# Kernel tuning notes

Hardware: AMD Instinct MI355X
Metric: run time of the kernel (lower is better)

The kernel has to match this reference:

```python
import jax, jax.numpy as jnp
import numpy as np

DIM = 768
N_HEADS = 12
HEAD_DIM = DIM // N_HEADS
MLP_MULT = 4
EPS = 1e-5


def setup_inputs() -> dict:
    key = jax.random.key(0)
    ks = jax.random.split(key, 8)
    B, T = 2, 4096
    s = lambda fan_in: 1.0 / np.sqrt(fan_in)
    return {
        "x": jax.random.normal(ks[0], (B, T, DIM), dtype=jnp.float32),
        "ln1_w": jnp.ones((DIM,), jnp.float32),
        "ln1_b": jnp.zeros((DIM,), jnp.float32),
        # weights stored as (in, out): y = x @ W + b (equivalent to torch Linear)
        "w_qkv": jax.random.normal(ks[1], (DIM, 3 * DIM), jnp.float32) * s(DIM),
        "w_proj": jax.random.normal(ks[2], (DIM, DIM), jnp.float32) * s(DIM),
        "b_proj": jnp.zeros((DIM,), jnp.float32),
        "ln2_w": jnp.ones((DIM,), jnp.float32),
        "ln2_b": jnp.zeros((DIM,), jnp.float32),
        "w1": jax.random.normal(ks[3], (DIM, MLP_MULT * DIM), jnp.float32) * s(DIM),
        "b1": jnp.zeros((MLP_MULT * DIM,), jnp.float32),
        "w2": jax.random.normal(ks[4], (MLP_MULT * DIM, DIM), jnp.float32) * s(MLP_MULT * DIM),
        "b2": jnp.zeros((DIM,), jnp.float32),
    }


def _layernorm(x, w, b):
    mean = jnp.mean(x, axis=-1, keepdims=True)
    var = jnp.var(x, axis=-1, keepdims=True)
    return w * (x - mean) * jax.lax.rsqrt(var + EPS) + b


def reference(x, ln1_w, ln1_b, w_qkv, w_proj, b_proj, ln2_w, ln2_b, w1, b1, w2, b2):
    B, T, C = x.shape
    scale = HEAD_DIM ** -0.5

    # --- attention sub-block (pre-LN) ---
    h = _layernorm(x, ln1_w, ln1_b)
    qkv = h @ w_qkv                               # [B, T, 3C]
    q, k, v = jnp.split(qkv, 3, axis=-1)
    to_heads = lambda t: t.reshape(B, T, N_HEADS, HEAD_DIM).transpose(0, 2, 1, 3)
    q, k, v = to_heads(q), to_heads(k), to_heads(v)  # [B, H, T, D]

    att = jnp.einsum("bhqd,bhkd->bhqk", q, k) * scale  # full T x T scores
    causal = jnp.tril(jnp.ones((T, T), dtype=bool))
    att = jnp.where(causal, att, -jnp.inf)
    att = jax.nn.softmax(att, axis=-1)
    y = jnp.einsum("bhqk,bhkd->bhqd", att, v)          # [B, H, T, D]
    y = y.transpose(0, 2, 1, 3).reshape(B, T, C)
    y = y @ w_proj + b_proj
    x = x + y

    # --- MLP sub-block (pre-LN) ---
    h = _layernorm(x, ln2_w, ln2_b)
    h = jax.nn.gelu(h @ w1 + b1, approximate=False)
    h = h @ w2 + b2
    return x + h
```

## Files before the change

### kernel.cpp

```cpp
#include <hip/hip_runtime.h>

typedef unsigned short u16;
typedef __attribute__((ext_vector_type(4))) unsigned short u16x4;
typedef __attribute__((ext_vector_type(8))) short short8;
typedef __attribute__((ext_vector_type(4))) float f32x4;
typedef __attribute__((ext_vector_type(16))) float f32x16;

#define MFMA32(a, b, c) __builtin_amdgcn_mfma_f32_32x32x16_bf16(a, b, c, 0, 0, 0)

__device__ __forceinline__ u16 f2bf(float f) {
  union { float f; unsigned u; } x; x.f = f;
  unsigned r = x.u + 0x7fffu + ((x.u >> 16) & 1u);
  return (u16)(r >> 16);
}

__device__ __forceinline__ unsigned cvt_pk_bf16(float lo, float hi) {
  unsigned r;
  asm("v_cvt_pk_bf16_f32 %0, %1, %2" : "=v"(r) : "v"(lo), "v"(hi));
  return r;
}

__device__ __forceinline__ float fexp2m8(float t) {
  union { int i; float f; } u;
  u.i = (int)__builtin_fmaf(t, 8388608.f, 997996889.f);
  return u.f;
}

__device__ __forceinline__ void load_lds16(const void* g, void* l) {
  __builtin_amdgcn_global_load_lds(
      (const __attribute__((address_space(1))) void*)g,
      (__attribute__((address_space(3))) void*)l,
      16, 0, 0);
}

__global__ __launch_bounds__(256) void prep_k(
    const float* __restrict__ wqkv, const float* __restrict__ wproj,
    const float* __restrict__ w1, const float* __restrict__ w2,
    u16* __restrict__ wqkvT, u16* __restrict__ wprojT,
    u16* __restrict__ w1T, u16* __restrict__ w2T,
    const float* __restrict__ x, const float* __restrict__ ln1w,
    const float* __restrict__ ln1b, u16* __restrict__ hbuf) {
  __shared__ float smem[32 * 33];
  const int bid = blockIdx.x;
  const int tid = threadIdx.x;
  if (bid < 6912) {
    const float* in; u16* out; int C, tb;
    int R;
    if (bid < 1728)      { in = wqkv;  out = wqkvT;  R = 768;  C = 2304; tb = bid; }
    else if (bid < 2304) { in = wproj; out = wprojT; R = 768;  C = 768;  tb = bid - 1728; }
    else if (bid < 4608) { in = w1;    out = w1T;    R = 768;  C = 3072; tb = bid - 2304; }
    else                 { in = w2;    out = w2T;    R = 3072; C = 768;  tb = bid - 4608; }
    const int nCt = C >> 5;
    const int c0 = (tb % nCt) * 32, r0 = (tb / nCt) * 32;
    const int tx = tid & 31, ty = tid >> 5;
    float (*tile)[33] = (float(*)[33])smem;
#pragma unroll
    for (int i = 0; i < 4; ++i)
      tile[ty + i * 8][tx] = in[(size_t)(r0 + ty + i * 8) * C + c0 + tx];
    __syncthreads();
#pragma unroll
    for (int i = 0; i < 4; ++i)
      out[(size_t)(c0 + ty + i * 8) * R + r0 + tx] = f2bf(tile[tx][ty + i * 8]);
  } else {
    const int row = bid - 6912;
    const float* xr = x + (size_t)row * 768;
    float v0 = xr[tid], v1 = xr[tid + 256], v2 = xr[tid + 512];
    float s = v0 + v1 + v2;
    float s2 = v0 * v0 + v1 * v1 + v2 * v2;
#pragma unroll
    for (int m = 32; m; m >>= 1) { s += __shfl_xor(s, m); s2 += __shfl_xor(s2, m); }
    float* ps = smem;
    float* ps2 = smem + 4;
    if ((tid & 63) == 0) { ps[tid >> 6] = s; ps2[tid >> 6] = s2; }
    __syncthreads();
    s = ps[0] + ps[1] + ps[2] + ps[3];
    s2 = ps2[0] + ps2[1] + ps2[2] + ps2[3];
    const float mean = s * (1.f / 768.f);
    const float var = s2 * (1.f / 768.f) - mean * mean;
    const float rstd = rsqrtf(var + 1e-5f);
    u16* orow = hbuf + (size_t)row * 768;
    orow[tid]       = f2bf((v0 - mean) * rstd * ln1w[tid]       + ln1b[tid]);
    orow[tid + 256] = f2bf((v1 - mean) * rstd * ln1w[tid + 256] + ln1b[tid + 256]);
    orow[tid + 512] = f2bf((v2 - mean) * rstd * ln1w[tid + 512] + ln1b[tid + 512]);
  }
}

__global__ __launch_bounds__(256) void ln_k(const float* __restrict__ X,
                                            const float* __restrict__ w,
                                            const float* __restrict__ b,
                                            u16* __restrict__ O) {
  const int row = blockIdx.x;
  const float* xr = X + (size_t)row * 768;
  const int tid = threadIdx.x;
  float v0 = xr[tid], v1 = xr[tid + 256], v2 = xr[tid + 512];
  float s = v0 + v1 + v2;
  float s2 = v0 * v0 + v1 * v1 + v2 * v2;
#pragma unroll
  for (int m = 32; m; m >>= 1) { s += __shfl_xor(s, m); s2 += __shfl_xor(s2, m); }
  __shared__ float ps[4], ps2[4];
  if ((tid & 63) == 0) { ps[tid >> 6] = s; ps2[tid >> 6] = s2; }
  __syncthreads();
  s = ps[0] + ps[1] + ps[2] + ps[3];
  s2 = ps2[0] + ps2[1] + ps2[2] + ps2[3];
  const float mean = s * (1.f / 768.f);
  const float var = s2 * (1.f / 768.f) - mean * mean;
  const float rstd = rsqrtf(var + 1e-5f);
  u16* orow = O + (size_t)row * 768;
  orow[tid]       = f2bf((v0 - mean) * rstd * w[tid]       + b[tid]);
  orow[tid + 256] = f2bf((v1 - mean) * rstd * w[tid + 256] + b[tid + 256]);
  orow[tid + 512] = f2bf((v2 - mean) * rstd * w[tid + 512] + b[tid + 512]);
}

#define BM 128
#define BN 128
#define BKK 64

template <int EPI>
__global__ __launch_bounds__(256, 3) void gemm_k(
    const u16* __restrict__ A, const u16* __restrict__ Bt, int K, int N,
    const float* __restrict__ bias, const float* __restrict__ res,
    float* __restrict__ outF, u16* __restrict__ outB,
    u16* __restrict__ qout, u16* __restrict__ kout, u16* __restrict__ vout) {
  __shared__ __align__(16) u16 sA[BM * BKK];
  __shared__ __align__(16) u16 sB[BN * BKK];
  const int nTn = N / BN;
  const int nwg = gridDim.x;
  const int bid = ((int)blockIdx.x & 7) * (nwg >> 3) + ((int)blockIdx.x >> 3);
  const int tm = bid / nTn, tn = bid % nTn;
  const int m0 = tm * BM, n0 = tn * BN;
  const int tid = threadIdx.x, lane = tid & 63, wv = tid >> 6;
  const int wr = wv >> 1, wc = wv & 1;
  const int fr = lane & 15, fg = lane >> 4;

  const u16* aSrc[4];
  const u16* bSrc[4];
#pragma unroll
  for (int i = 0; i < 4; ++i) {
    int f = (i * 4 + wv) * 64 + lane;
    int r = f >> 3;
    int c = (f & 7) ^ (r & 7);
    aSrc[i] = A + (size_t)(m0 + r) * K + c * 8;
    bSrc[i] = Bt + (size_t)(n0 + r) * K + c * 8;
  }

  f32x4 acc[4][4];
#pragma unroll
  for (int m = 0; m < 4; ++m)
#pragma unroll
    for (int n = 0; n < 4; ++n) acc[m][n] = f32x4{0.f, 0.f, 0.f, 0.f};

  const int aswz = fr & 7;
  for (int kt = 0; kt < K; kt += BKK) {
#pragma unroll
    for (int i = 0; i < 4; ++i) {
      load_lds16(aSrc[i] + kt, (char*)sA + (i * 4 + wv) * 1024);
      load_lds16(bSrc[i] + kt, (char*)sB + (i * 4 + wv) * 1024);
    }
    __syncthreads();
#pragma unroll
    for (int ks = 0; ks < 2; ++ks) {
      const int c16 = (ks * 4 + fg) ^ aswz;
      short8 af[4], bf[4];
#pragma unroll
      for (int m = 0; m < 4; ++m)
        af[m] = *(const short8*)((const char*)sA +
                                 (((wr * 64 + m * 16 + fr) * 8 + c16) << 4));
#pragma unroll
      for (int n = 0; n < 4; ++n)
        bf[n] = *(const short8*)((const char*)sB +
                                 (((wc * 64 + n * 16 + fr) * 8 + c16) << 4));
#pragma unroll
      for (int m = 0; m < 4; ++m)
#pragma unroll
        for (int n = 0; n < 4; ++n)
          acc[m][n] =
              __builtin_amdgcn_mfma_f32_16x16x32_bf16(af[m], bf[n], acc[m][n], 0, 0, 0);
    }
    __syncthreads();
  }

#pragma unroll
  for (int m = 0; m < 4; ++m) {
    const int row = m0 + wr * 64 + m * 16 + fg * 4;
#pragma unroll
    for (int n = 0; n < 4; ++n) {
      const int col = n0 + wc * 64 + n * 16 + fr;
      f32x4 v = acc[m][n];
      if (EPI == 0) {
        const int part = (col >= 1536) ? 2 : (col >= 768 ? 1 : 0);
        const int cc = col - part * 768;
        const int hh = cc >> 6, dd = cc & 63;
        const int bb = row >> 12;
        const int t = row & 4095;
        const size_t bhh = (size_t)(bb * 12 + hh);
        if (part == 2) {
          const int ks_ = (t & 63) >> 4, h_ = (t >> 3) & 1, e0 = t & 7;
          u16x4 pk = {f2bf(v[0]), f2bf(v[1]), f2bf(v[2]), f2bf(v[3])};
          *(u16x4*)(vout + bhh * 262144 + (size_t)(t >> 6) * 4096 +
                    (size_t)(((ks_ << 2) + ((dd >> 5) << 1) + h_) * 256 +
                             (dd & 31) * 8 + e0)) = pk;
        } else if (part == 1) {
          const int ks_ = dd >> 4, h_ = (dd >> 3) & 1, e = dd & 7;
          u16* base = kout + bhh * 262144;
#pragma unroll
          for (int r = 0; r < 4; ++r) {
            const int t2 = t + r;
            base[(size_t)(t2 >> 6) * 4096 +
                 (size_t)((((ks_ << 2) + (((t2 & 63) >> 5) << 1) + h_) * 256) +
                          (t2 & 31) * 8 + e)] = f2bf(v[r]);
          }
        } else {
          const float qs = 0.18033688011112042f;
          u16* dst = qout + (bhh * 4096 + t) * 64 + dd;
#pragma unroll
          for (int r = 0; r < 4; ++r) dst[(size_t)r * 64] = f2bf(v[r] * qs);
        }
      } else if (EPI == 1) {
        const float bv = bias[col];
#pragma unroll
        for (int r = 0; r < 4; ++r)
          outF[(size_t)(row + r) * N + col] =
              v[r] + bv + res[(size_t)(row + r) * N + col];
      } else {
        const float bv = bias[col];
#pragma unroll
        for (int r = 0; r < 4; ++r) {
          float t = v[r] + bv;
          float g = 0.5f * t * (1.f + erff(t * 0.70710678118654752f));
          outB[(size_t)(row + r) * N + col] = f2bf(g);
        }
      }
    }
  }
}

__global__ __launch_bounds__(256, 4) void gemm64_k(
    const u16* __restrict__ A, const u16* __restrict__ Bt, int K, int N,
    const float* __restrict__ bias, const float* __restrict__ res,
    float* __restrict__ outF) {
  __shared__ __align__(16) u16 sA[128 * 64];
  __shared__ __align__(16) u16 sB[64 * 64];
  const int nTn = N / 64;
  const int nwg = gridDim.x;
  const int bid = ((int)blockIdx.x & 7) * (nwg >> 3) + ((int)blockIdx.x >> 3);
  const int tm = bid / nTn, tn = bid % nTn;
  const int m0 = tm * 128, n0 = tn * 64;
  const int tid = threadIdx.x, lane = tid & 63, wv = tid >> 6;
  const int fr = lane & 15, fg = lane >> 4;

  const u16* aSrc[4];
  const u16* bSrc[2];
#pragma unroll
  for (int i = 0; i < 4; ++i) {
    const int f = i * 256 + tid;
    const int r = f >> 3;
    const int c = (f & 7) ^ (r & 7);
    aSrc[i] = A + (size_t)(m0 + r) * K + c * 8;
  }
#pragma unroll
  for (int i = 0; i < 2; ++i) {
    const int f = i * 256 + tid;
    const int r = f >> 3;
    const int c = (f & 7) ^ (r & 7);
    bSrc[i] = Bt + (size_t)(n0 + r) * K + c * 8;
  }

  f32x4 acc[2][4];
#pragma unroll
  for (int m = 0; m < 2; ++m)
#pragma unroll
    for (int n = 0; n < 4; ++n) acc[m][n] = f32x4{0.f, 0.f, 0.f, 0.f};

  const int aswz = fr & 7;
  for (int kt = 0; kt < K; kt += 64) {
#pragma unroll
    for (int i = 0; i < 4; ++i)
      load_lds16(aSrc[i] + kt, (char*)sA + (i * 256 + tid) * 16);
#pragma unroll
    for (int i = 0; i < 2; ++i)
      load_lds16(bSrc[i] + kt, (char*)sB + (i * 256 + tid) * 16);
    __syncthreads();
#pragma unroll
    for (int ks = 0; ks < 2; ++ks) {
      const int c16 = (ks * 4 + fg) ^ aswz;
      short8 af[2], bf[4];
#pragma unroll
      for (int m = 0; m < 2; ++m)
        af[m] = *(const short8*)((const char*)sA +
                                 (((wv * 32 + m * 16 + fr) * 8 + c16) << 4));
#pragma unroll
      for (int n = 0; n < 4; ++n)
        bf[n] = *(const short8*)((const char*)sB +
                                 (((n * 16 + fr) * 8 + c16) << 4));
#pragma unroll
      for (int m = 0; m < 2; ++m)
#pragma unroll
        for (int n = 0; n < 4; ++n)
          acc[m][n] =
              __builtin_amdgcn_mfma_f32_16x16x32_bf16(af[m], bf[n], acc[m][n], 0, 0, 0);
    }
    __syncthreads();
  }

#pragma unroll
  for (int m = 0; m < 2; ++m) {
    const int row = m0 + wv * 32 + m * 16 + fg * 4;
#pragma unroll
    for (int n = 0; n < 4; ++n) {
      const int col = n0 + n * 16 + fr;
      const float bv = bias[col];
      f32x4 v = acc[m][n];
#pragma unroll
      for (int r = 0; r < 4; ++r)
        outF[(size_t)(row + r) * N + col] =
            v[r] + bv + res[(size_t)(row + r) * N + col];
    }
  }
}

__global__ __launch_bounds__(256, 3) void attn_k(const u16* __restrict__ Q,
                                                 const u16* __restrict__ Kb,
                                                 const u16* __restrict__ Vt,
                                                 u16* __restrict__ Y) {
  __shared__ __align__(16) u16 sK[2][8192];
  __shared__ __align__(16) u16 sV[8192];
  const int b = blockIdx.x;
  const int c255 = b & 255, slot = b >> 8;
  const int rank = (slot == 0) ? c255 : (slot == 1 ? 511 - c255 : 512 + c255);
  const int qt = 31 - rank / 24;
  const int bh = rank % 24;
  const int bb = bh / 12, hh = bh - bb * 12;
  const int tid = threadIdx.x, lane = tid & 63, wv = tid >> 6;
  const int l31 = lane & 31, hi = lane >> 5;
  const int wq0 = qt * 128 + wv * 32;
  const int qG = wq0 + l31;
  const u16* Qh = Q + (size_t)bh * 262144;
  const u16* Kh = Kb + (size_t)bh * 262144;
  const u16* Vh = Vt + (size_t)bh * 262144;

  short8 qf[4];
#pragma unroll
  for (int ks = 0; ks < 4; ++ks)
    qf[ks] = *(const short8*)(Qh + (size_t)qG * 64 + ks * 16 + hi * 8);

  const short8 onesf = {(short)0x3F80, (short)0x3F80, (short)0x3F80,
                        (short)0x3F80, (short)0x3F80, (short)0x3F80,
                        (short)0x3F80, (short)0x3F80};

  f32x16 yacc[2];
  yacc[0] = (f32x16)0.f;
  yacc[1] = (f32x16)0.f;
  f32x16 lsum = (f32x16)0.f;

#define STAGE_K(buf, cc)                                                       \
  do {                                                                         \
    const u16* gk_ = Kh + (size_t)(cc)*8192;                                   \
    _Pragma("unroll") for (int i_ = 0; i_ < 4; ++i_) {                         \
      const int f_ = i_ * 256 + tid;                                           \
      load_lds16(gk_ + f_ * 8, (char*)sK[buf] + f_ * 16);                      \
    }                                                                          \
  } while (0)

#define STAGE_V(cc)                                                            \
  do {                                                                         \
    const u16* gv_ = Vh + (size_t)(cc)*8192;                                   \
    _Pragma("unroll") for (int i_ = 0; i_ < 4; ++i_) {                         \
      const int f_ = i_ * 256 + tid;                                           \
      load_lds16(gv_ + f_ * 8, (char*)sV + f_ * 16);                           \
    }                                                                          \
  } while (0)

  const int nch = qt + 1;
  STAGE_K(0, 0);
  __syncthreads();

  const int rdBase = hi * 512 + l31 * 16;

  for (int c = 0; c < nch; ++c) {
    const int cur = c & 1;
    STAGE_V(c);
    if (c + 1 < nch) STAGE_K(cur ^ 1, c + 1);

    const bool act1 = (c * 128 + 64) <= (wq0 + 31);

    unsigned pw[2][16];
#pragma unroll
    for (int hf = 0; hf < 2; ++hf) {
      if (hf == 0 || act1) {
        const int kb = c * 128 + hf * 64;
        const char* sKb = (const char*)sK[cur] + hf * 8192;

        f32x16 s[2];
        s[0] = (f32x16)0.f;
        s[1] = (f32x16)0.f;
        __builtin_amdgcn_s_setprio(1);
#pragma unroll
        for (int ks = 0; ks < 4; ++ks) {
#pragma unroll
          for (int kc = 0; kc < 2; ++kc) {
            short8 kf = *(const short8*)(sKb + ks * 2048 + kc * 1024 + rdBase);
            s[kc] = MFMA32(kf, qf[ks], s[kc]);
          }
        }
        __builtin_amdgcn_s_setprio(0);

        if (kb + 63 > wq0) {
#pragma unroll
          for (int kc = 0; kc < 2; ++kc)
#pragma unroll
            for (int r = 0; r < 16; ++r) {
              const int key = kb + kc * 32 + (r & 3) + 8 * (r >> 2) + 4 * hi;
              if (key > qG) s[kc][r] = -110.f;
            }
        }

#pragma unroll
        for (int kc = 0; kc < 2; ++kc)
#pragma unroll
          for (int r = 0; r < 16; ++r)
            s[kc][r] = fexp2m8(s[kc][r]);

#pragma unroll
        for (int ks2 = 0; ks2 < 4; ++ks2) {
          const int kc = ks2 >> 1, rb = (ks2 & 1) * 8;
          unsigned W0 = cvt_pk_bf16(s[kc][rb + 0], s[kc][rb + 1]);
          unsigned W1 = cvt_pk_bf16(s[kc][rb + 2], s[kc][rb + 3]);
          unsigned W2 = cvt_pk_bf16(s[kc][rb + 4], s[kc][rb + 5]);
          unsigned W3 = cvt_pk_bf16(s[kc][rb + 6], s[kc][rb + 7]);
          asm("v_permlane32_swap_b32 %0, %1" : "+v"(W0), "+v"(W2));
          asm("v_permlane32_swap_b32 %0, %1" : "+v"(W1), "+v"(W3));
          pw[hf][ks2 * 4 + 0] = W0;
          pw[hf][ks2 * 4 + 1] = W1;
          pw[hf][ks2 * 4 + 2] = W2;
          pw[hf][ks2 * 4 + 3] = W3;
        }
      }
    }

    __syncthreads();

#pragma unroll
    for (int hf = 0; hf < 2; ++hf) {
      if (hf == 0 || act1) {
        const char* sVb = (const char*)sV + hf * 8192;
        __builtin_amdgcn_s_setprio(1);
#pragma unroll
        for (int ks2 = 0; ks2 < 4; ++ks2) {
          union { unsigned w[4]; short8 v; } pb;
          pb.w[0] = pw[hf][ks2 * 4 + 0];
          pb.w[1] = pw[hf][ks2 * 4 + 1];
          pb.w[2] = pw[hf][ks2 * 4 + 2];
          pb.w[3] = pw[hf][ks2 * 4 + 3];
#pragma unroll
          for (int dt = 0; dt < 2; ++dt) {
            short8 vf = *(const short8*)(sVb + ks2 * 2048 + dt * 1024 + rdBase);
            yacc[dt] = MFMA32(vf, pb.v, yacc[dt]);
          }
          lsum = MFMA32(onesf, pb.v, lsum);
        }
        __builtin_amdgcn_s_setprio(0);
      }
    }
    __syncthreads();
  }

  const float inv = 1.f / lsum[0];
  u16* Yr = Y + (size_t)(bb * 4096 + qt * 128 + wv * 32 + l31) * 768 + hh * 64;
#pragma unroll
  for (int dt = 0; dt < 2; ++dt)
#pragma unroll
    for (int g = 0; g < 4; ++g) {
      u16x4 pk = {f2bf(yacc[dt][g * 4 + 0] * inv), f2bf(yacc[dt][g * 4 + 1] * inv),
                  f2bf(yacc[dt][g * 4 + 2] * inv), f2bf(yacc[dt][g * 4 + 3] * inv)};
      *(u16x4*)(Yr + dt * 32 + g * 8 + hi * 4) = pk;
    }
#undef STAGE_K
#undef STAGE_V
}

extern "C" void kernel_launch(void* const* d_in, const int* in_sizes, int n_in,
                              void* d_out, int out_size, void* d_ws, size_t ws_size,
                              hipStream_t stream) {
  const float* x = (const float*)d_in[0];
  const float* ln1w = (const float*)d_in[1];
  const float* ln1b = (const float*)d_in[2];
  const float* wqkv = (const float*)d_in[3];
  const float* wproj = (const float*)d_in[4];
  const float* bproj = (const float*)d_in[5];
  const float* ln2w = (const float*)d_in[6];
  const float* ln2b = (const float*)d_in[7];
  const float* w1 = (const float*)d_in[8];
  const float* b1 = (const float*)d_in[9];
  const float* w2 = (const float*)d_in[10];
  const float* b2 = (const float*)d_in[11];
  float* out = (float*)d_out;
  char* ws = (char*)d_ws;

  const size_t SZ_ACT = (size_t)8192 * 768 * 2;
  u16* hbuf = (u16*)(ws);
  u16* qb = (u16*)(ws + SZ_ACT);
  u16* kb = (u16*)(ws + 2 * SZ_ACT);
  u16* vT = (u16*)(ws + 3 * SZ_ACT);
  u16* ybuf = (u16*)(ws + 4 * SZ_ACT);
  float* out1 = (float*)(ws + 5 * SZ_ACT);
  char* wsw = ws + 5 * SZ_ACT + (size_t)8192 * 768 * 4;
  u16* wqkvT = (u16*)(wsw);
  u16* wprojT = (u16*)(wsw + 3538944);
  u16* w1T = (u16*)(wsw + 3538944 + 1179648);
  u16* w2T = (u16*)(wsw + 3538944 + 1179648 + 4718592);
  u16* h3 = hbuf;
  u16* h2 = ybuf;

  prep_k<<<15104, 256, 0, stream>>>(wqkv, wproj, w1, w2,
                                    wqkvT, wprojT, w1T, w2T,
                                    x, ln1w, ln1b, hbuf);

  gemm_k<0><<<64 * (2304 / 128), 256, 0, stream>>>(hbuf, wqkvT, 768, 2304,
      nullptr, nullptr, nullptr, nullptr, qb, kb, vT);

  attn_k<<<768, 256, 0, stream>>>(qb, kb, vT, ybuf);

  gemm64_k<<<64 * (768 / 64), 256, 0, stream>>>(ybuf, wprojT, 768, 768,
      bproj, x, out1);

  ln_k<<<8192, 256, 0, stream>>>(out1, ln2w, ln2b, h2);

  gemm_k<2><<<64 * (3072 / 128), 256, 0, stream>>>(h2, w1T, 768, 3072,
      b1, nullptr, nullptr, h3, nullptr, nullptr, nullptr);

  gemm64_k<<<64 * (768 / 64), 256, 0, stream>>>(h3, w2T, 3072, 768,
      b2, out1, out);

  (void)in_sizes; (void)n_in; (void)out_size; (void)ws_size;
}
```

Baseline: 248.3 us.

## Overlap next-tile global-to-LDS loads with MFMA compute in GEMM kernels

```diff
diff --git a/kernel.cpp b/kernel.cpp
--- a/kernel.cpp
+++ b/kernel.cpp
@@ -143,6 +143,14 @@
     bSrc[i] = Bt + (size_t)(n0 + r) * K + c * 8;
   }
 
+#define GSTAGE(kt)                                                             \
+  do {                                                                         \
+    _Pragma("unroll") for (int i_ = 0; i_ < 4; ++i_) {                         \
+      load_lds16(aSrc[i_] + (kt), (char*)sA + (i_ * 4 + wv) * 1024);           \
+      load_lds16(bSrc[i_] + (kt), (char*)sB + (i_ * 4 + wv) * 1024);           \
+    }                                                                          \
+  } while (0)
+
   f32x4 acc[4][4];
 #pragma unroll
   for (int m = 0; m < 4; ++m)
@@ -150,34 +158,37 @@
     for (int n = 0; n < 4; ++n) acc[m][n] = f32x4{0.f, 0.f, 0.f, 0.f};
 
   const int aswz = fr & 7;
-  for (int kt = 0; kt < K; kt += BKK) {
-#pragma unroll
-    for (int i = 0; i < 4; ++i) {
-      load_lds16(aSrc[i] + kt, (char*)sA + (i * 4 + wv) * 1024);
-      load_lds16(bSrc[i] + kt, (char*)sB + (i * 4 + wv) * 1024);
-    }
-    __syncthreads();
+  const int nkt = K / BKK;
+  GSTAGE(0);
+  __syncthreads();
+
+  for (int t = 0; t < nkt; ++t) {
+    short8 af[2][4], bf[2][4];
 #pragma unroll
     for (int ks = 0; ks < 2; ++ks) {
       const int c16 = (ks * 4 + fg) ^ aswz;
-      short8 af[4], bf[4];
 #pragma unroll
       for (int m = 0; m < 4; ++m)
-        af[m] = *(const short8*)((const char*)sA +
-                                 (((wr * 64 + m * 16 + fr) * 8 + c16) << 4));
+        af[ks][m] = *(const short8*)((const char*)sA +
+                                     (((wr * 64 + m * 16 + fr) * 8 + c16) << 4));
 #pragma unroll
       for (int n = 0; n < 4; ++n)
-        bf[n] = *(const short8*)((const char*)sB +
-                                 (((wc * 64 + n * 16 + fr) * 8 + c16) << 4));
+        bf[ks][n] = *(const short8*)((const char*)sB +
+                                     (((wc * 64 + n * 16 + fr) * 8 + c16) << 4));
+    }
+    __syncthreads();
+    if (t + 1 < nkt) GSTAGE((t + 1) * BKK);
+#pragma unroll
+    for (int ks = 0; ks < 2; ++ks)
 #pragma unroll
       for (int m = 0; m < 4; ++m)
 #pragma unroll
         for (int n = 0; n < 4; ++n)
-          acc[m][n] =
-              __builtin_amdgcn_mfma_f32_16x16x32_bf16(af[m], bf[n], acc[m][n], 0, 0, 0);
-    }
-    __syncthreads();
-  }
+          acc[m][n] = __builtin_amdgcn_mfma_f32_16x16x32_bf16(af[ks][m], bf[ks][n],
+                                                              acc[m][n], 0, 0, 0);
+    __syncthreads();
+  }
+#undef GSTAGE
 
 #pragma unroll
   for (int m = 0; m < 4; ++m) {
@@ -265,6 +276,14 @@
     bSrc[i] = Bt + (size_t)(n0 + r) * K + c * 8;
   }
 
+#define GSTAGE64(kt)                                                           \
+  do {                                                                         \
+    _Pragma("unroll") for (int i_ = 0; i_ < 4; ++i_)                           \
+        load_lds16(aSrc[i_] + (kt), (char*)sA + (i_ * 256 + tid) * 16);        \
+    _Pragma("unroll") for (int i_ = 0; i_ < 2; ++i_)                           \
+        load_lds16(bSrc[i_] + (kt), (char*)sB + (i_ * 256 + tid) * 16);        \
+  } while (0)
+
   f32x4 acc[2][4];
 #pragma unroll
   for (int m = 0; m < 2; ++m)
@@ -272,35 +291,37 @@
     for (int n = 0; n < 4; ++n) acc[m][n] = f32x4{0.f, 0.f, 0.f, 0.f};
 
   const int aswz = fr & 7;
-  for (int kt = 0; kt < K; kt += 64) {
-#pragma unroll
-    for (int i = 0; i < 4; ++i)
-      load_lds16(aSrc[i] + kt, (char*)sA + (i * 256 + tid) * 16);
-#pragma unroll
-    for (int i = 0; i < 2; ++i)
-      load_lds16(bSrc[i] + kt, (char*)sB + (i * 256 + tid) * 16);
-    __syncthreads();
+  const int nkt = K / 64;
+  GSTAGE64(0);
+  __syncthreads();
+
+  for (int t = 0; t < nkt; ++t) {
+    short8 af[2][2], bf[2][4];
 #pragma unroll
     for (int ks = 0; ks < 2; ++ks) {
       const int c16 = (ks * 4 + fg) ^ aswz;
-      short8 af[2], bf[4];
 #pragma unroll
       for (int m = 0; m < 2; ++m)
-        af[m] = *(const short8*)((const char*)sA +
-                                 (((wv * 32 + m * 16 + fr) * 8 + c16) << 4));
+        af[ks][m] = *(const short8*)((const char*)sA +
+                                     (((wv * 32 + m * 16 + fr) * 8 + c16) << 4));
 #pragma unroll
       for (int n = 0; n < 4; ++n)
-        bf[n] = *(const short8*)((const char*)sB +
-                                 (((n * 16 + fr) * 8 + c16) << 4));
+        bf[ks][n] = *(const short8*)((const char*)sB +
+                                     (((n * 16 + fr) * 8 + c16) << 4));
+    }
+    __syncthreads();
+    if (t + 1 < nkt) GSTAGE64((t + 1) * 64);
+#pragma unroll
+    for (int ks = 0; ks < 2; ++ks)
 #pragma unroll
       for (int m = 0; m < 2; ++m)
 #pragma unroll
         for (int n = 0; n < 4; ++n)
-          acc[m][n] =
-              __builtin_amdgcn_mfma_f32_16x16x32_bf16(af[m], bf[n], acc[m][n], 0, 0, 0);
-    }
-    __syncthreads();
-  }
+          acc[m][n] = __builtin_amdgcn_mfma_f32_16x16x32_bf16(af[ks][m], bf[ks][n],
+                                                              acc[m][n], 0, 0, 0);
+    __syncthreads();
+  }
+#undef GSTAGE64
 
 #pragma unroll
   for (int m = 0; m < 2; ++m) {
```

After: 247.4 us. Within noise of the previous version (-0.4%).
